# Optimization experiments

Hardware: AMD Instinct MI355X
Metric: run time of the kernel (lower is better)

Reference implementation:

```python
import jax, jax.numpy as jnp
import numpy as np

SLOPE = 25.0  # fast_sigmoid surrogate slope
THR = 1.0     # snntorch Leaky default threshold

@jax.custom_vjp
def spike(x):
    # heaviside forward, fast-sigmoid surrogate backward
    return (x > 0).astype(x.dtype)

def _spike_fwd(x):
    return spike(x), x

def _spike_bwd(x, g):
    return (g / (SLOPE * jnp.abs(x) + 1.0) ** 2,)

spike.defvjp(_spike_fwd, _spike_bwd)


def _xavier(k, shape):
    fan_out, fan_in = shape
    lim = np.sqrt(6.0 / (fan_in + fan_out)).astype(np.float32)
    return jax.random.uniform(k, shape, jnp.float32, -lim, lim)


def setup_inputs() -> dict:
    key = jax.random.key(0)
    ks = jax.random.split(key, 6)
    B, T, NI, H1, H2, NO = 256, 100, 512, 1024, 1024, 10
    return {
        "x": jax.random.normal(ks[0], (B, T, NI), jnp.float32),
        "W1": _xavier(ks[1], (H1, NI)),
        "W1r": _xavier(ks[2], (H1, H1)),
        "W2": _xavier(ks[3], (H2, H1)),
        "W2r": _xavier(ks[4], (H2, H2)),
        "Wout": _xavier(ks[5], (NO, H2)),
        "beta1": jnp.float32(0.9),
        "beta2": jnp.float32(0.9),
        "beta_out": jnp.float32(0.9),
    }


def reference(x, W1, W1r, W2, W2r, Wout, beta1, beta2, beta_out):
    B, T, NI = x.shape
    H1, H2, NO = W1.shape[0], W2.shape[0], Wout.shape[0]
    b1 = jnp.clip(beta1, 0.0, 1.0)
    b2 = jnp.clip(beta2, 0.0, 1.0)
    bo = jnp.clip(beta_out, 0.0, 1.0)
    xt = jnp.transpose(x, (1, 0, 2))  # [T, B, NI]

    def step(carry, x_t):
        mem1, spk1, mem2, spk2, mem_out = carry
        # layer 1: feedforward + recurrent current, leaky integrate, subtract-reset
        cur1 = x_t @ W1.T + spk1 @ W1r.T
        reset1 = jax.lax.stop_gradient((mem1 > THR).astype(mem1.dtype))
        mem1 = b1 * mem1 + cur1 - reset1 * THR
        spk1 = spike(mem1 - THR)
        # layer 2
        cur2 = spk1 @ W2.T + spk2 @ W2r.T
        reset2 = jax.lax.stop_gradient((mem2 > THR).astype(mem2.dtype))
        mem2 = b2 * mem2 + cur2 - reset2 * THR
        spk2 = spike(mem2 - THR)
        # readout: reset_mechanism='none'
        mem_out = bo * mem_out + spk2 @ Wout.T
        return (mem1, spk1, mem2, spk2, mem_out), (spk1, mem_out)

    z = lambda n: jnp.zeros((B, n), x.dtype)
    carry0 = (z(H1), z(H1), z(H2), z(H2), z(NO))
    _, (spk1_rec, mem_out_rec) = jax.lax.scan(step, carry0, xt)
    return spk1_rec, mem_out_rec  # [T,B,H1], [T,B,NO]
```

## Files before the change

### kernel.cpp

```cpp
#include <hip/hip_runtime.h>

#define S_ELE (256 * 1024)
#define NBLK 512
#define GRP  8
#define GSZ  (NBLK / GRP)

typedef float f32x4 __attribute__((ext_vector_type(4)));

struct Ptrs {
    const float *x, *W1, *W1r, *W2, *W2r, *Wout;
    const float *b1, *b2, *bo;
    float *spk1_rec, *mout_rec;
    float *mem1, *mem2, *memo;
    float *w1rt, *w2t, *w2rt, *xw, *S2;
    unsigned *bar, *cnt1, *cnt2;
    unsigned short *idx1, *idx2;
    int t_ch;
};

__device__ __forceinline__ float clip01(float b) { return fminf(fmaxf(b, 0.0f), 1.0f); }
__device__ __forceinline__ float4 ld4(const float* p) { return *reinterpret_cast<const float4*>(p); }
__device__ __forceinline__ void   st4(float* p, float4 v) { *reinterpret_cast<float4*>(p) = v; }
__device__ __forceinline__ void   st4nt(float* p, float4 v)
{
    f32x4 n = { v.x, v.y, v.z, v.w };
    __builtin_nontemporal_store(n, reinterpret_cast<f32x4*>(p));
}

__device__ __forceinline__ float4 memup(float4 mo, float4 cur, float b, float4* sv)
{
    float4 mn, s;
    mn.x = b * mo.x + cur.x - (mo.x > 1.0f ? 1.0f : 0.0f); s.x = (mn.x - 1.0f) > 0.0f ? 1.0f : 0.0f;
    mn.y = b * mo.y + cur.y - (mo.y > 1.0f ? 1.0f : 0.0f); s.y = (mn.y - 1.0f) > 0.0f ? 1.0f : 0.0f;
    mn.z = b * mo.z + cur.z - (mo.z > 1.0f ? 1.0f : 0.0f); s.z = (mn.z - 1.0f) > 0.0f ? 1.0f : 0.0f;
    mn.w = b * mo.w + cur.w - (mo.w > 1.0f ? 1.0f : 0.0f); s.w = (mn.w - 1.0f) > 0.0f ? 1.0f : 0.0f;
    *sv = s; return mn;
}

__device__ __forceinline__ void gbar(unsigned* bar)
{
    __syncthreads();
    if (threadIdx.x == 0) {
        unsigned g = __hip_atomic_load(&bar[0], __ATOMIC_RELAXED, __HIP_MEMORY_SCOPE_AGENT);
        unsigned* gc = &bar[8 + (blockIdx.x & (GRP - 1)) * 32];
        unsigned a = __hip_atomic_fetch_add(gc, 1u, __ATOMIC_ACQ_REL, __HIP_MEMORY_SCOPE_AGENT);
        if (a == GSZ - 1) {
            __hip_atomic_store(gc, 0u, __ATOMIC_RELAXED, __HIP_MEMORY_SCOPE_AGENT);
            unsigned tp = __hip_atomic_fetch_add(&bar[1], 1u, __ATOMIC_ACQ_REL, __HIP_MEMORY_SCOPE_AGENT);
            if (tp == GRP - 1) {
                __hip_atomic_store(&bar[1], 0u, __ATOMIC_RELAXED, __HIP_MEMORY_SCOPE_AGENT);
                __hip_atomic_store(&bar[0], g + 1u, __ATOMIC_RELEASE, __HIP_MEMORY_SCOPE_AGENT);
            }
        }
        while (__hip_atomic_load(&bar[0], __ATOMIC_ACQUIRE, __HIP_MEMORY_SCOPE_AGENT) == g)
            __builtin_amdgcn_s_sleep(2);
    }
    __syncthreads();
}

__device__ __forceinline__ void tr32(float* sm, const float* src, float* dst, int tr, int tc)
{
    const int t = (int)threadIdx.x;
    const int r = t >> 3, c4 = (t & 7) << 2;
    __syncthreads();
    float4 v = ld4(src + (size_t)(tr * 32 + r) * 1024 + tc * 32 + c4);
    sm[r * 33 + c4 + 0] = v.x; sm[r * 33 + c4 + 1] = v.y;
    sm[r * 33 + c4 + 2] = v.z; sm[r * 33 + c4 + 3] = v.w;
    __syncthreads();
    const int kk = t >> 3, nn4 = (t & 7) << 2;
    float4 o;
    o.x = sm[(nn4 + 0) * 33 + kk]; o.y = sm[(nn4 + 1) * 33 + kk];
    o.z = sm[(nn4 + 2) * 33 + kk]; o.w = sm[(nn4 + 3) * 33 + kk];
    st4(dst + (size_t)(tc * 32 + kk) * 1024 + tr * 32 + nn4, o);
}

__device__ __forceinline__ void xw_tile(float* sm, const float* xA, const float* W1,
                                        float* out, int tm, int tn)
{
    float* As = sm;
    float* Bs = sm + 1056;
    const int t = (int)threadIdx.x;
    const int ar = t >> 1;
    const int ak = (t & 1) << 2;
    const int r0 = (t >> 4) << 3;
    const int c0 = (t & 15) << 3;
    const float* Ab = xA + (size_t)(tm * 128) * 51200;
    const float* Bb = W1 + (size_t)(tn * 128) * 512;
    float4 pa = ld4(Ab + (size_t)ar * 51200 + ak);
    float4 pb = ld4(Bb + (size_t)ar * 512 + ak);
    float acc[8][8] = {};
    for (int c = 0; c < 64; ++c) {
        __syncthreads();
        As[(ak + 0) * 132 + ar] = pa.x; As[(ak + 1) * 132 + ar] = pa.y;
        As[(ak + 2) * 132 + ar] = pa.z; As[(ak + 3) * 132 + ar] = pa.w;
        Bs[(ak + 0) * 132 + ar] = pb.x; Bs[(ak + 1) * 132 + ar] = pb.y;
        Bs[(ak + 2) * 132 + ar] = pb.z; Bs[(ak + 3) * 132 + ar] = pb.w;
        __syncthreads();
        if (c + 1 < 64) {
            const int ko = (c + 1) * 8;
            pa = ld4(Ab + (size_t)ar * 51200 + ko + ak);
            pb = ld4(Bb + (size_t)ar * 512 + ko + ak);
        }
        #pragma unroll
        for (int k = 0; k < 8; ++k) {
            float4 a0 = ld4(&As[k * 132 + r0]);
            float4 a1 = ld4(&As[k * 132 + r0 + 4]);
            float4 b0 = ld4(&Bs[k * 132 + c0]);
            float4 b1 = ld4(&Bs[k * 132 + c0 + 4]);
            float av[8] = {a0.x, a0.y, a0.z, a0.w, a1.x, a1.y, a1.z, a1.w};
            float bv[8] = {b0.x, b0.y, b0.z, b0.w, b1.x, b1.y, b1.z, b1.w};
            #pragma unroll
            for (int i = 0; i < 8; ++i)
                #pragma unroll
                for (int j = 0; j < 8; ++j)
                    acc[i][j] = fmaf(av[i], bv[j], acc[i][j]);
        }
    }
    #pragma unroll
    for (int i = 0; i < 8; ++i) {
        float* row = out + (size_t)(tm * 128 + r0 + i) * 1024 + tn * 128 + c0;
        st4(row,     make_float4(acc[i][0], acc[i][1], acc[i][2], acc[i][3]));
        st4(row + 4, make_float4(acc[i][4], acc[i][5], acc[i][6], acc[i][7]));
    }
}

template <int NC>
__device__ __forceinline__ void gatherN(const unsigned short* const lp[],
    const unsigned st[], const unsigned en[], const float* Wt, int n4, float4 c[])
{
    unsigned j[NC], e[NC];
    float4 pa[NC], pb[NC];
    #pragma unroll
    for (int q = 0; q < NC; ++q) {
        j[q] = st[q]; e[q] = en[q];
        c[q] = make_float4(0.f, 0.f, 0.f, 0.f);
        if (j[q] < e[q])     pa[q] = ld4(Wt + (size_t)lp[q][j[q]] * 1024 + n4);
        if (j[q] + 1 < e[q]) pb[q] = ld4(Wt + (size_t)lp[q][j[q] + 1] * 1024 + n4);
    }
    for (;;) {
        bool any = false;
        #pragma unroll
        for (int q = 0; q < NC; ++q) {
            if (j[q] < e[q]) {
                float4 v = pa[q];
                pa[q] = pb[q];
                if (j[q] + 2 < e[q]) pb[q] = ld4(Wt + (size_t)lp[q][j[q] + 2] * 1024 + n4);
                c[q].x += v.x; c[q].y += v.y; c[q].z += v.z; c[q].w += v.w;
                ++j[q];
                any = any || (j[q] < e[q]);
            }
        }
        if (!any) break;
    }
}

__device__ __forceinline__ void build_list(const float* s_spk,
    unsigned short* gidx, unsigned* gcnt)
{
    const int l = (int)threadIdx.x;
    unsigned tot = 0, prev = 0;
    #pragma unroll
    for (int i = 0; i < 16; ++i) {
        float s = s_spk[i * 64 + l];
        unsigned long long m = __ballot(s != 0.0f);
        unsigned off = (unsigned)__popcll(m & ((1ull << l) - 1ull));
        if (s != 0.0f) gidx[tot + off] = (unsigned short)(i * 64 + l);
        tot += (unsigned)__popcll(m);
        if (i & 1) { if (l == 0) gcnt[i >> 1] = tot - prev; prev = tot; }
    }
}

__device__ __forceinline__ void l1_full(float* sm, const Ptrs& p, int r, int tau)
{
    const int t = (int)threadIdx.x, n4 = t << 2;
    const int pp = 1 - (tau & 1);
    const unsigned* cw = p.cnt1 + ((size_t)pp * 256 + r) * 8;
    unsigned pos[9];
    pos[0] = 0;
    #pragma unroll
    for (int w = 0; w < 8; ++w) pos[w + 1] = pos[w] + cw[w];
    unsigned* sl = (unsigned*)(sm + 1024);
    const unsigned* gl = (const unsigned*)(p.idx1 + ((size_t)pp * 256 + r) * 1024);
    for (unsigned i = t; i < ((pos[8] + 1) >> 1); i += 256) sl[i] = gl[i];
    __syncthreads();
    const unsigned short* sl16 = (const unsigned short*)sl;
    const unsigned short* lp[8];
    unsigned st[8], en[8];
    #pragma unroll
    for (int q = 0; q < 8; ++q) { lp[q] = sl16; st[q] = pos[q]; en[q] = pos[q + 1]; }
    float4 c[8];
    gatherN<8>(lp, st, en, p.w1rt, n4, c);

    const size_t base = (size_t)r * 1024 + n4;
    const int slot = tau % p.t_ch;
    float4 acc = ld4(p.xw + (size_t)slot * S_ELE + base);
    #pragma unroll
    for (int w = 0; w < 8; ++w) {
        acc.x += c[w].x; acc.y += c[w].y; acc.z += c[w].z; acc.w += c[w].w;
    }
    const float bb = clip01(*p.b1);
    float4 mo = ld4(p.mem1 + base);
    float4 sv; float4 mn = memup(mo, acc, bb, &sv);
    st4(p.mem1 + base, mn);
    st4nt(p.spk1_rec + (size_t)tau * S_ELE + base, sv);
    sm[n4 + 0] = sv.x; sm[n4 + 1] = sv.y; sm[n4 + 2] = sv.z; sm[n4 + 3] = sv.w;
    __syncthreads();
    if (t < 64) build_list(sm, p.idx1 + ((size_t)(tau & 1) * 256 + r) * 1024,
                           p.cnt1 + ((size_t)(tau & 1) * 256 + r) * 8);
}

__device__ __forceinline__ void l2g(float* sm, const Ptrs& p, int idx, int rsel, int step)
{
    const int t = (int)threadIdx.x, n4 = t << 2;
    const int r0 = idx * 2, r1 = r0 + 1;
    const int par = rsel ? (1 - (step & 1)) : (step & 1);
    const unsigned* cbase = (rsel ? p.cnt2 : p.cnt1) + (size_t)par * 256 * 8;
    const unsigned short* ibase = (rsel ? p.idx2 : p.idx1) + (size_t)par * 256 * 1024;
    const unsigned* cA = cbase + (size_t)r0 * 8;
    const unsigned* cB = cbase + (size_t)r1 * 8;
    unsigned nlo0 = cA[0] + cA[1] + cA[2] + cA[3];
    unsigned tot0 = nlo0 + cA[4] + cA[5] + cA[6] + cA[7];
    unsigned nlo1 = cB[0] + cB[1] + cB[2] + cB[3];
    unsigned tot1 = nlo1 + cB[4] + cB[5] + cB[6] + cB[7];
    unsigned* sl0 = (unsigned*)(sm + 1024);
    unsigned* sl1 = (unsigned*)(sm + 1536);
    const unsigned* g0 = (const unsigned*)(ibase + (size_t)r0 * 1024);
    const unsigned* g1 = (const unsigned*)(ibase + (size_t)r1 * 1024);
    for (unsigned i = t; i < ((tot0 + 1) >> 1); i += 256) sl0[i] = g0[i];
    for (unsigned i = t; i < ((tot1 + 1) >> 1); i += 256) sl1[i] = g1[i];
    __syncthreads();
    const unsigned short* lp[4] = {(const unsigned short*)sl0, (const unsigned short*)sl0,
                                   (const unsigned short*)sl1, (const unsigned short*)sl1};
    unsigned st[4] = {0, nlo0, 0, nlo1};
    unsigned en[4] = {nlo0, tot0, nlo1, tot1};
    float4 c[4];
    gatherN<4>(lp, st, en, rsel ? p.w2rt : p.w2t, n4, c);
    float* Sp = p.S2 + (size_t)rsel * S_ELE;
    st4(Sp + (size_t)r0 * 1024 + n4,
        make_float4(c[0].x + c[1].x, c[0].y + c[1].y, c[0].z + c[1].z, c[0].w + c[1].w));
    st4(Sp + (size_t)r1 * 1024 + n4,
        make_float4(c[2].x + c[3].x, c[2].y + c[3].y, c[2].z + c[3].z, c[2].w + c[3].w));
}

__device__ __forceinline__ void upd2_row(float* sm, const Ptrs& p, int r, int step)
{
    const int t = (int)threadIdx.x, n4 = t << 2;
    const size_t base = (size_t)r * 1024 + n4;
    float4 sa = ld4(p.S2 + base);
    float4 sb = ld4(p.S2 + (size_t)S_ELE + base);
    float4 cur = make_float4(sa.x + sb.x, sa.y + sb.y, sa.z + sb.z, sa.w + sb.w);
    const float bb = clip01(*p.b2);
    float4 mo = ld4(p.mem2 + base);
    float4 sv; float4 mn = memup(mo, cur, bb, &sv);
    st4(p.mem2 + base, mn);
    sm[n4 + 0] = sv.x; sm[n4 + 1] = sv.y; sm[n4 + 2] = sv.z; sm[n4 + 3] = sv.w;
    __syncthreads();
    if (t < 64) build_list(sm, p.idx2 + ((size_t)(step & 1) * 256 + r) * 1024,
                           p.cnt2 + ((size_t)(step & 1) * 256 + r) * 8);
    const int wave = t >> 6, lane = t & 63;
    const float bo = clip01(*p.bo);
    float v[16];
    #pragma unroll
    for (int i = 0; i < 16; ++i) v[i] = sm[lane + 64 * i];
    float* rec = p.mout_rec + (size_t)step * 2560;
    for (int o = wave; o < 10; o += 4) {
        float sum = 0.0f;
        #pragma unroll
        for (int i = 0; i < 16; ++i)
            sum = fmaf(v[i], p.Wout[o * 1024 + lane + 64 * i], sum);
        #pragma unroll
        for (int off = 32; off > 0; off >>= 1) sum += __shfl_down(sum, off);
        if (lane == 0) {
            const float m = bo * p.memo[r * 10 + o] + sum;
            p.memo[r * 10 + o] = m;
            __builtin_nontemporal_store(m, &rec[r * 10 + o]);
        }
    }
}

__global__ __launch_bounds__(256, 2) void snn_all(Ptrs p)
{
    __shared__ float sm[2176];
    const int bid = (int)blockIdx.x;
    const int x = bid & 7, g = bid >> 3;

    for (int task = bid; task < 3072; task += NBLK) {
        const float* src = task < 1024 ? p.W1r : (task < 2048 ? p.W2 : p.W2r);
        float* dst = task < 1024 ? p.w1rt : (task < 2048 ? p.w2t : p.w2rt);
        const int id = task & 1023;
        tr32(sm, src, dst, id >> 5, id & 31);
    }
    gbar(p.bar);

    for (int tau = 0; tau <= 100; ++tau) {
        if (tau < 100 && (tau % p.t_ch) == 0) {
            const int ntask = p.t_ch * 16;
            for (int task = bid; task < ntask; task += NBLK) {
                const int tp = task >> 4, tile = task & 15;
                xw_tile(sm, p.x + (size_t)(tau + tp) * 512, p.W1,
                        p.xw + (size_t)tp * S_ELE, tile >> 3, tile & 7);
            }
            gbar(p.bar);
        }
        if (x < 4)      { if (tau < 100) l1_full(sm, p, g * 4 + x, tau); }
        else if (x < 6) { if (tau >= 1)  l2g(sm, p, g * 2 + (x - 4), 0, tau - 1); }
        else            { if (tau >= 1)  l2g(sm, p, g * 2 + (x - 6), 1, tau - 1); }
        gbar(p.bar);
        if (x >= 4 && tau >= 1) upd2_row(sm, p, g * 4 + (x - 4), tau - 1);
        gbar(p.bar);
    }
}

__global__ __launch_bounds__(256, 2) void fb_pre(Ptrs p)
{
    __shared__ float sm[2176];
    for (int task = blockIdx.x; task < 3072; task += gridDim.x) {
        const float* src = task < 1024 ? p.W1r : (task < 2048 ? p.W2 : p.W2r);
        float* dst = task < 1024 ? p.w1rt : (task < 2048 ? p.w2t : p.w2rt);
        const int id = task & 1023;
        tr32(sm, src, dst, id >> 5, id & 31);
    }
}

__global__ __launch_bounds__(256, 2) void fb_xw(Ptrs p, int t0)
{
    __shared__ float sm[2176];
    const int task = (int)blockIdx.x;
    const int tp = task >> 4, tile = task & 15;
    xw_tile(sm, p.x + (size_t)(t0 + tp) * 512, p.W1,
            p.xw + (size_t)tp * S_ELE, tile >> 3, tile & 7);
}

__global__ __launch_bounds__(256, 2) void fb_p1(Ptrs p, int tau)
{
    __shared__ float sm[2176];
    const int bid = (int)blockIdx.x;
    const int x = bid & 7, g = bid >> 3;
    if (x < 4)      { if (tau < 100) l1_full(sm, p, g * 4 + x, tau); }
    else if (x < 6) { if (tau >= 1)  l2g(sm, p, g * 2 + (x - 4), 0, tau - 1); }
    else            { if (tau >= 1)  l2g(sm, p, g * 2 + (x - 6), 1, tau - 1); }
}

__global__ __launch_bounds__(256, 2) void fb_p2(Ptrs p, int tau)
{
    __shared__ float sm[2176];
    if (tau >= 1) upd2_row(sm, p, (int)blockIdx.x, tau - 1);
}

extern "C" void kernel_launch(void* const* d_in, const int* in_sizes, int n_in,
                              void* d_out, int out_size, void* d_ws, size_t ws_size,
                              hipStream_t stream)
{
    Ptrs p;
    p.x    = (const float*)d_in[0];
    p.W1   = (const float*)d_in[1];
    p.W1r  = (const float*)d_in[2];
    p.W2   = (const float*)d_in[3];
    p.W2r  = (const float*)d_in[4];
    p.Wout = (const float*)d_in[5];
    p.b1   = (const float*)d_in[6];
    p.b2   = (const float*)d_in[7];
    p.bo   = (const float*)d_in[8];

    float* out = (float*)d_out;
    p.spk1_rec = out;
    p.mout_rec = out + (size_t)100 * S_ELE;

    float* w = (float*)d_ws;
    p.mem1 = w;  w += S_ELE;
    p.mem2 = w;  w += S_ELE;
    p.memo = w;  w += 2560;
    p.bar  = (unsigned*)w;  w += 512;
    p.cnt1 = (unsigned*)w;  w += 4096;
    p.cnt2 = (unsigned*)w;  w += 4096;
    p.idx1 = (unsigned short*)w;  w += 262144;
    p.idx2 = (unsigned short*)w;  w += 262144;
    p.w1rt = w;  w += 1048576;
    p.w2t  = w;  w += 1048576;
    p.w2rt = w;  w += 1048576;
    p.S2   = w;  w += 2 * S_ELE;
    p.xw   = w;

    const size_t used = (size_t)(w - (float*)d_ws) * sizeof(float);
    int t_ch = 1;
    const int cands[] = {100, 50, 25, 20, 10, 5, 4, 2, 1};
    for (int c : cands)
        if (used + (size_t)c * S_ELE * sizeof(float) <= ws_size) { t_ch = c; break; }
    p.t_ch = t_ch;

    (void)hipMemsetAsync(p.mem1, 0,
                   ((size_t)2 * S_ELE + 2560 + 512 + 8192) * sizeof(float), stream);

    int maxb = 0;
    hipError_t qerr = hipOccupancyMaxActiveBlocksPerMultiprocessor(
        &maxb, (const void*)snn_all, 256, 0);
    bool coop = (qerr == hipSuccess && maxb >= 2);

    if (coop) {
        void* args[] = { (void*)&p };
        if (hipLaunchCooperativeKernel((const void*)snn_all, dim3(NBLK), dim3(256),
                                       args, 0, stream) != hipSuccess)
            coop = false;
    }

    if (!coop) {
        hipLaunchKernelGGL(fb_pre, dim3(NBLK), dim3(256), 0, stream, p);
        for (int tau = 0; tau <= 100; ++tau) {
            if (tau < 100 && (tau % t_ch) == 0)
                hipLaunchKernelGGL(fb_xw, dim3(t_ch * 16), dim3(256), 0, stream, p, tau);
            hipLaunchKernelGGL(fb_p1, dim3(NBLK), dim3(256), 0, stream, p, tau);
            hipLaunchKernelGGL(fb_p2, dim3(256), dim3(256), 0, stream, p, tau);
        }
    }
}
```

Baseline: 4.527 ms.

## Balance sparse gather work across all blocks and use hierarchical barrier release

```diff
diff --git a/kernel.cpp b/kernel.cpp
--- a/kernel.cpp
+++ b/kernel.cpp
@@ -12,7 +12,7 @@
     const float *b1, *b2, *bo;
     float *spk1_rec, *mout_rec;
     float *mem1, *mem2, *memo;
-    float *w1rt, *w2t, *w2rt, *xw, *S2;
+    float *w1rt, *w2t, *w2rt, *xw, *P1, *S2;
     unsigned *bar, *cnt1, *cnt2;
     unsigned short *idx1, *idx2;
     int t_ch;
@@ -41,8 +41,9 @@
 {
     __syncthreads();
     if (threadIdx.x == 0) {
+        const int grp = (int)blockIdx.x & (GRP - 1);
         unsigned g = __hip_atomic_load(&bar[0], __ATOMIC_RELAXED, __HIP_MEMORY_SCOPE_AGENT);
-        unsigned* gc = &bar[8 + (blockIdx.x & (GRP - 1)) * 32];
+        unsigned* gc = &bar[8 + grp * 32];
         unsigned a = __hip_atomic_fetch_add(gc, 1u, __ATOMIC_ACQ_REL, __HIP_MEMORY_SCOPE_AGENT);
         if (a == GSZ - 1) {
             __hip_atomic_store(gc, 0u, __ATOMIC_RELAXED, __HIP_MEMORY_SCOPE_AGENT);
@@ -52,8 +53,15 @@
                 __hip_atomic_store(&bar[0], g + 1u, __ATOMIC_RELEASE, __HIP_MEMORY_SCOPE_AGENT);
             }
         }
-        while (__hip_atomic_load(&bar[0], __ATOMIC_ACQUIRE, __HIP_MEMORY_SCOPE_AGENT) == g)
-            __builtin_amdgcn_s_sleep(2);
+        unsigned* mir = &bar[256 + grp * 32];
+        if (a == 0) {
+            while (__hip_atomic_load(&bar[0], __ATOMIC_ACQUIRE, __HIP_MEMORY_SCOPE_AGENT) == g)
+                __builtin_amdgcn_s_sleep(2);
+            __hip_atomic_store(mir, g + 1u, __ATOMIC_RELEASE, __HIP_MEMORY_SCOPE_AGENT);
+        } else {
+            while (__hip_atomic_load(mir, __ATOMIC_ACQUIRE, __HIP_MEMORY_SCOPE_AGENT) < g + 1u)
+                __builtin_amdgcn_s_sleep(2);
+        }
     }
     __syncthreads();
 }
@@ -124,27 +132,27 @@
     }
 }
 
-template <int NC>
-__device__ __forceinline__ void gatherN(const unsigned short* const lp[],
-    const unsigned st[], const unsigned en[], const float* Wt, int n4, float4 c[])
-{
-    unsigned j[NC], e[NC];
-    float4 pa[NC], pb[NC];
-    #pragma unroll
-    for (int q = 0; q < NC; ++q) {
+__device__ __forceinline__ void gather6(const unsigned short* const lst[6],
+    const unsigned st[6], const unsigned en[6], const float* const wt[6],
+    int n4, float4 c[6])
+{
+    unsigned j[6], e[6];
+    float4 pa[6], pb[6];
+    #pragma unroll
+    for (int q = 0; q < 6; ++q) {
         j[q] = st[q]; e[q] = en[q];
         c[q] = make_float4(0.f, 0.f, 0.f, 0.f);
-        if (j[q] < e[q])     pa[q] = ld4(Wt + (size_t)lp[q][j[q]] * 1024 + n4);
-        if (j[q] + 1 < e[q]) pb[q] = ld4(Wt + (size_t)lp[q][j[q] + 1] * 1024 + n4);
+        if (j[q] < e[q])     pa[q] = ld4(wt[q] + (size_t)lst[q][j[q]] * 1024 + n4);
+        if (j[q] + 1 < e[q]) pb[q] = ld4(wt[q] + (size_t)lst[q][j[q] + 1] * 1024 + n4);
     }
     for (;;) {
         bool any = false;
         #pragma unroll
-        for (int q = 0; q < NC; ++q) {
+        for (int q = 0; q < 6; ++q) {
             if (j[q] < e[q]) {
                 float4 v = pa[q];
                 pa[q] = pb[q];
-                if (j[q] + 2 < e[q]) pb[q] = ld4(Wt + (size_t)lp[q][j[q] + 2] * 1024 + n4);
+                if (j[q] + 2 < e[q]) pb[q] = ld4(wt[q] + (size_t)lst[q][j[q] + 2] * 1024 + n4);
                 c[q].x += v.x; c[q].y += v.y; c[q].z += v.z; c[q].w += v.w;
                 ++j[q];
                 any = any || (j[q] < e[q]);
@@ -170,33 +178,78 @@
     }
 }
 
-__device__ __forceinline__ void l1_full(float* sm, const Ptrs& p, int r, int tau)
-{
+__device__ __forceinline__ void phase1(const Ptrs& p, int bid, int tau)
+{
+    const int x = bid & 7, g = bid >> 3;
     const int t = (int)threadIdx.x, n4 = t << 2;
-    const int pp = 1 - (tau & 1);
-    const unsigned* cw = p.cnt1 + ((size_t)pp * 256 + r) * 8;
-    unsigned pos[9];
-    pos[0] = 0;
-    #pragma unroll
-    for (int w = 0; w < 8; ++w) pos[w + 1] = pos[w] + cw[w];
-    unsigned* sl = (unsigned*)(sm + 1024);
-    const unsigned* gl = (const unsigned*)(p.idx1 + ((size_t)pp * 256 + r) * 1024);
-    for (unsigned i = t; i < ((pos[8] + 1) >> 1); i += 256) sl[i] = gl[i];
-    __syncthreads();
-    const unsigned short* sl16 = (const unsigned short*)sl;
-    const unsigned short* lp[8];
-    unsigned st[8], en[8];
-    #pragma unroll
-    for (int q = 0; q < 8; ++q) { lp[q] = sl16; st[q] = pos[q]; en[q] = pos[q + 1]; }
-    float4 c[8];
-    gatherN<8>(lp, st, en, p.w1rt, n4, c);
-
+
+    const unsigned short* lst[6];
+    const float* wt[6];
+    unsigned st[6], en[6];
+    #pragma unroll
+    for (int q = 0; q < 6; ++q) { lst[q] = p.idx1; wt[q] = p.w1rt; st[q] = 0; en[q] = 0; }
+
+    if (tau < 100) {
+        const int pp = 1 - (tau & 1);
+        #pragma unroll
+        for (int q = 0; q < 4; ++q) {
+            const int r = 4 * g + q;
+            const unsigned* cw = p.cnt1 + ((size_t)pp * 256 + r) * 8;
+            unsigned s0 = 0;
+            for (int w = 0; w < x; ++w) s0 += cw[w];
+            st[q] = s0; en[q] = s0 + cw[x];
+            lst[q] = p.idx1 + ((size_t)pp * 256 + r) * 1024;
+            wt[q] = p.w1rt;
+        }
+    }
+    if (tau >= 1) {
+        const int s = tau - 1;
+        const int fam = x >> 1;
+        const int h = x & 1;
+        const int par = (fam < 2) ? (s & 1) : (1 - (s & 1));
+        const unsigned* cb = (fam < 2 ? p.cnt1 : p.cnt2) + (size_t)par * 256 * 8;
+        const unsigned short* ib = (fam < 2 ? p.idx1 : p.idx2) + (size_t)par * 256 * 1024;
+        const float* W = (fam < 2) ? p.w2t : p.w2rt;
+        const bool hi = (fam & 1);
+        #pragma unroll
+        for (int q = 4; q < 6; ++q) {
+            const int r = 128 * h + 2 * g + (q - 4);
+            const unsigned* cw = cb + (size_t)r * 8;
+            unsigned nlo = cw[0] + cw[1] + cw[2] + cw[3];
+            unsigned tot = nlo + cw[4] + cw[5] + cw[6] + cw[7];
+            st[q] = hi ? nlo : 0; en[q] = hi ? tot : nlo;
+            lst[q] = ib + (size_t)r * 1024;
+            wt[q] = W;
+        }
+    }
+
+    float4 c[6];
+    gather6(lst, st, en, wt, n4, c);
+
+    if (tau < 100) {
+        #pragma unroll
+        for (int q = 0; q < 4; ++q)
+            st4(p.P1 + (size_t)x * S_ELE + (size_t)(4 * g + q) * 1024 + n4, c[q]);
+    }
+    if (tau >= 1) {
+        const int plane = x >> 1, h = x & 1;
+        #pragma unroll
+        for (int q = 4; q < 6; ++q)
+            st4(p.S2 + (size_t)plane * S_ELE
+                     + (size_t)(128 * h + 2 * g + (q - 4)) * 1024 + n4, c[q]);
+    }
+}
+
+__device__ __forceinline__ void upd1_row(float* sm, const Ptrs& p, int r, int tau)
+{
+    const int t = (int)threadIdx.x, n4 = t << 2;
     const size_t base = (size_t)r * 1024 + n4;
     const int slot = tau % p.t_ch;
     float4 acc = ld4(p.xw + (size_t)slot * S_ELE + base);
     #pragma unroll
     for (int w = 0; w < 8; ++w) {
-        acc.x += c[w].x; acc.y += c[w].y; acc.z += c[w].z; acc.w += c[w].w;
+        float4 q = ld4(p.P1 + (size_t)w * S_ELE + base);
+        acc.x += q.x; acc.y += q.y; acc.z += q.z; acc.w += q.w;
     }
     const float bb = clip01(*p.b1);
     float4 mo = ld4(p.mem1 + base);
@@ -209,46 +262,19 @@
                            p.cnt1 + ((size_t)(tau & 1) * 256 + r) * 8);
 }
 
-__device__ __forceinline__ void l2g(float* sm, const Ptrs& p, int idx, int rsel, int step)
-{
-    const int t = (int)threadIdx.x, n4 = t << 2;
-    const int r0 = idx * 2, r1 = r0 + 1;
-    const int par = rsel ? (1 - (step & 1)) : (step & 1);
-    const unsigned* cbase = (rsel ? p.cnt2 : p.cnt1) + (size_t)par * 256 * 8;
-    const unsigned short* ibase = (rsel ? p.idx2 : p.idx1) + (size_t)par * 256 * 1024;
-    const unsigned* cA = cbase + (size_t)r0 * 8;
-    const unsigned* cB = cbase + (size_t)r1 * 8;
-    unsigned nlo0 = cA[0] + cA[1] + cA[2] + cA[3];
-    unsigned tot0 = nlo0 + cA[4] + cA[5] + cA[6] + cA[7];
-    unsigned nlo1 = cB[0] + cB[1] + cB[2] + cB[3];
-    unsigned tot1 = nlo1 + cB[4] + cB[5] + cB[6] + cB[7];
-    unsigned* sl0 = (unsigned*)(sm + 1024);
-    unsigned* sl1 = (unsigned*)(sm + 1536);
-    const unsigned* g0 = (const unsigned*)(ibase + (size_t)r0 * 1024);
-    const unsigned* g1 = (const unsigned*)(ibase + (size_t)r1 * 1024);
-    for (unsigned i = t; i < ((tot0 + 1) >> 1); i += 256) sl0[i] = g0[i];
-    for (unsigned i = t; i < ((tot1 + 1) >> 1); i += 256) sl1[i] = g1[i];
-    __syncthreads();
-    const unsigned short* lp[4] = {(const unsigned short*)sl0, (const unsigned short*)sl0,
-                                   (const unsigned short*)sl1, (const unsigned short*)sl1};
-    unsigned st[4] = {0, nlo0, 0, nlo1};
-    unsigned en[4] = {nlo0, tot0, nlo1, tot1};
-    float4 c[4];
-    gatherN<4>(lp, st, en, rsel ? p.w2rt : p.w2t, n4, c);
-    float* Sp = p.S2 + (size_t)rsel * S_ELE;
-    st4(Sp + (size_t)r0 * 1024 + n4,
-        make_float4(c[0].x + c[1].x, c[0].y + c[1].y, c[0].z + c[1].z, c[0].w + c[1].w));
-    st4(Sp + (size_t)r1 * 1024 + n4,
-        make_float4(c[2].x + c[3].x, c[2].y + c[3].y, c[2].z + c[3].z, c[2].w + c[3].w));
-}
-
 __device__ __forceinline__ void upd2_row(float* sm, const Ptrs& p, int r, int step)
 {
     const int t = (int)threadIdx.x, n4 = t << 2;
     const size_t base = (size_t)r * 1024 + n4;
-    float4 sa = ld4(p.S2 + base);
-    float4 sb = ld4(p.S2 + (size_t)S_ELE + base);
-    float4 cur = make_float4(sa.x + sb.x, sa.y + sb.y, sa.z + sb.z, sa.w + sb.w);
+    float4 p0 = ld4(p.S2 + base);
+    float4 p1 = ld4(p.S2 + (size_t)S_ELE + base);
+    float4 p2 = ld4(p.S2 + (size_t)2 * S_ELE + base);
+    float4 p3 = ld4(p.S2 + (size_t)3 * S_ELE + base);
+    float4 cur;
+    cur.x = (p0.x + p1.x) + (p2.x + p3.x);
+    cur.y = (p0.y + p1.y) + (p2.y + p3.y);
+    cur.z = (p0.z + p1.z) + (p2.z + p3.z);
+    cur.w = (p0.w + p1.w) + (p2.w + p3.w);
     const float bb = clip01(*p.b2);
     float4 mo = ld4(p.mem2 + base);
     float4 sv; float4 mn = memup(mo, cur, bb, &sv);
@@ -282,7 +308,6 @@
 {
     __shared__ float sm[2176];
     const int bid = (int)blockIdx.x;
-    const int x = bid & 7, g = bid >> 3;
 
     for (int task = bid; task < 3072; task += NBLK) {
         const float* src = task < 1024 ? p.W1r : (task < 2048 ? p.W2 : p.W2r);
@@ -302,11 +327,10 @@
             }
             gbar(p.bar);
         }
-        if (x < 4)      { if (tau < 100) l1_full(sm, p, g * 4 + x, tau); }
-        else if (x < 6) { if (tau >= 1)  l2g(sm, p, g * 2 + (x - 4), 0, tau - 1); }
-        else            { if (tau >= 1)  l2g(sm, p, g * 2 + (x - 6), 1, tau - 1); }
+        phase1(p, bid, tau);
         gbar(p.bar);
-        if (x >= 4 && tau >= 1) upd2_row(sm, p, g * 4 + (x - 4), tau - 1);
+        if (bid < 256)      { if (tau < 100) upd1_row(sm, p, bid, tau); }
+        else                { if (tau >= 1)  upd2_row(sm, p, bid - 256, tau - 1); }
         gbar(p.bar);
     }
 }
@@ -333,18 +357,15 @@
 
 __global__ __launch_bounds__(256, 2) void fb_p1(Ptrs p, int tau)
 {
+    phase1(p, (int)blockIdx.x, tau);
+}
+
+__global__ __launch_bounds__(256, 2) void fb_p2(Ptrs p, int tau)
+{
     __shared__ float sm[2176];
     const int bid = (int)blockIdx.x;
-    const int x = bid & 7, g = bid >> 3;
-    if (x < 4)      { if (tau < 100) l1_full(sm, p, g * 4 + x, tau); }
-    else if (x < 6) { if (tau >= 1)  l2g(sm, p, g * 2 + (x - 4), 0, tau - 1); }
-    else            { if (tau >= 1)  l2g(sm, p, g * 2 + (x - 6), 1, tau - 1); }
-}
-
-__global__ __launch_bounds__(256, 2) void fb_p2(Ptrs p, int tau)
-{
-    __shared__ float sm[2176];
-    if (tau >= 1) upd2_row(sm, p, (int)blockIdx.x, tau - 1);
+    if (bid < 256)      { if (tau < 100) upd1_row(sm, p, bid, tau); }
+    else                { if (tau >= 1)  upd2_row(sm, p, bid - 256, tau - 1); }
 }
 
 extern "C" void kernel_launch(void* const* d_in, const int* in_sizes, int n_in,
@@ -378,7 +399,8 @@
     p.w1rt = w;  w += 1048576;
     p.w2t  = w;  w += 1048576;
     p.w2rt = w;  w += 1048576;
-    p.S2   = w;  w += 2 * S_ELE;
+    p.P1   = w;  w += 8 * S_ELE;
+    p.S2   = w;  w += 4 * S_ELE;
     p.xw   = w;
 
     const size_t used = (size_t)(w - (float*)d_ws) * sizeof(float);
@@ -409,7 +431,7 @@
             if (tau < 100 && (tau % t_ch) == 0)
                 hipLaunchKernelGGL(fb_xw, dim3(t_ch * 16), dim3(256), 0, stream, p, tau);
             hipLaunchKernelGGL(fb_p1, dim3(NBLK), dim3(256), 0, stream, p, tau);
-            hipLaunchKernelGGL(fb_p2, dim3(256), dim3(256), 0, stream, p, tau);
-        }
-    }
-}
+            hipLaunchKernelGGL(fb_p2, dim3(NBLK), dim3(256), 0, stream, p, tau);
+        }
+    }
+}
```

After: 6.264 ms. +38.4%, slower.
